# Performance work log

Hardware: AMD Instinct MI355X
Metric: run time of the kernel (lower is better)

## Reference

```python
import jax, jax.numpy as jnp
import numpy as np

HEAD_DIM = 128
ROPE_THETA = 10000.0


def _rope_cos_sin(positions, head_dim, theta):
    # positions: [T] int -> cos/sin [T, head_dim] (LLaMA half-split convention)
    inv_freq = 1.0 / (theta ** (jnp.arange(0, head_dim, 2, dtype=jnp.float32) / head_dim))
    ang = positions.astype(jnp.float32)[:, None] * inv_freq  # [T, D/2]
    cos = jnp.concatenate([jnp.cos(ang), jnp.cos(ang)], axis=-1)
    sin = jnp.concatenate([jnp.sin(ang), jnp.sin(ang)], axis=-1)
    return cos, sin


def _apply_rope(x, cos, sin):
    # x: [T, H, D]; rotate_half: (-x2, x1)
    half = x.shape[-1] // 2
    rot = jnp.concatenate([-x[..., half:], x[..., :half]], axis=-1)
    return x * cos[:, None, :] + rot * sin[:, None, :]


def setup_inputs() -> dict:
    key = jax.random.key(0)
    ks = jax.random.split(key, 5)
    T, hid = 4096, 4096
    S = 1024  # equal-length sequences -> B = T // S = 4
    Hq, Hk, D = 32, 8, HEAD_DIM
    hidden = jax.random.normal(ks[0], (T, hid), dtype=jnp.float32)
    positions = (jnp.arange(T, dtype=jnp.int32) % S)
    q_w = jax.random.normal(ks[1], (Hq * D, hid), dtype=jnp.float32) * 0.02
    k_w = jax.random.normal(ks[2], (Hk * D, hid), dtype=jnp.float32) * 0.02
    v_w = jax.random.normal(ks[3], (Hk * D, hid), dtype=jnp.float32) * 0.02
    o_w = jax.random.normal(ks[4], (hid, Hq * D), dtype=jnp.float32) * 0.02
    return {"hidden": hidden, "positions": positions, "q_w": q_w, "k_w": k_w,
            "v_w": v_w, "o_w": o_w, "seq_len": S}


def reference(hidden, positions, q_w, k_w, v_w, o_w, seq_len):
    T, hid = hidden.shape
    D = HEAD_DIM
    Hq = q_w.shape[0] // D
    Hk = k_w.shape[0] // D
    G = Hq // Hk  # num_kv_groups
    S = int(seq_len)
    B = T // S
    # QKV projections (ColumnParallel, tp=1): y = x @ W^T
    q = (hidden @ q_w.T).reshape(T, Hq, D)
    k = (hidden @ k_w.T).reshape(T, Hk, D)
    v = (hidden @ v_w.T).reshape(T, Hk, D)
    # fused RoPE on q and k
    cos, sin = _rope_cos_sin(positions, D, ROPE_THETA)
    q = _apply_rope(q, cos, sin)
    k = _apply_rope(k, cos, sin)
    # varlen (equal-length) causal GQA attention
    q = q.reshape(B, S, Hk, G, D)
    k = k.reshape(B, S, Hk, D)
    v = v.reshape(B, S, Hk, D)
    scale = 1.0 / np.sqrt(D).astype(np.float32)
    scores = jnp.einsum('bqhgd,bkhd->bhgqk', q, k) * scale  # [B,Hk,G,S,S]
    causal = jnp.tril(jnp.ones((S, S), dtype=bool))
    scores = jnp.where(causal, scores, jnp.asarray(-1e30, scores.dtype))
    attn = jax.nn.softmax(scores, axis=-1)
    out = jnp.einsum('bhgqk,bkhd->bqhgd', attn, v).reshape(T, Hq * D)
    # output projection (RowParallel, tp=1)
    return out @ o_w.T
```

## Files before the change

### kernel.cpp

```cpp
#include <hip/hip_runtime.h>
#include <hip/hip_bf16.h>

typedef __attribute__((ext_vector_type(8))) short bf16x8;
typedef __attribute__((ext_vector_type(4))) float f32x4;
typedef __attribute__((ext_vector_type(8))) unsigned short u16x8;

__device__ inline unsigned short f2bf(float f) {
  unsigned u = __builtin_bit_cast(unsigned, f);
  u += 0x7FFFu + ((u >> 16) & 1u);
  return (unsigned short)(u >> 16);
}
__device__ inline float b2f(unsigned short h) {
  unsigned u = ((unsigned)h) << 16;
  return __builtin_bit_cast(float, u);
}

typedef const __attribute__((address_space(1))) void* gas_ptr;
typedef __attribute__((address_space(3))) void* las_ptr;
__device__ inline void load_lds16(const void* g, void* l) {
  __builtin_amdgcn_global_load_lds((gas_ptr)g, (las_ptr)l, 16, 0, 0);
}

#define PHB() do { asm volatile("" ::: "memory"); __builtin_amdgcn_s_barrier(); \
                   __builtin_amdgcn_sched_barrier(0); } while (0)

__global__ __launch_bounds__(256) void cvt_f32_bf16(const float* __restrict__ src,
                                                    unsigned short* __restrict__ dst,
                                                    int n4) {
  int i = blockIdx.x * 256 + threadIdx.x;
  if (i >= n4) return;
  float4 v = ((const float4*)src)[i];
  ushort4 o;
  o.x = f2bf(v.x); o.y = f2bf(v.y); o.z = f2bf(v.z); o.w = f2bf(v.w);
  ((ushort4*)dst)[i] = o;
}

template <int NLOADS>
__device__ inline void stage_tile(const unsigned short* __restrict__ g, int ld,
                                  size_t grow0, int kcol0, char* ldsdst, int tid) {
#pragma unroll
  for (int i = 0; i < NLOADS; ++i) {
    int c = tid + i * 512;
    int r = c >> 3;
    int k = (c & 7) ^ (r & 7);
    load_lds16(g + (grow0 + r) * ld + kcol0 + k * 8, ldsdst + c * 16);
  }
}

__device__ inline void xcd_decode(int orig, int nTM, int nTN, int& bm, int& bn) {
  int x = orig & 7, i = orig >> 3;
  int xr = x >> 1, xc = x & 1;
  int bmch = nTM >> 2, bnch = nTN >> 1;
  bm = xr * bmch + i / bnch;
  bn = xc * bnch + i % bnch;
}

template <int Kc, int Nc, int Mc, bool OUT_F32>
__global__ __launch_bounds__(512, 1) void gemmT(const unsigned short* __restrict__ A,
                                                const unsigned short* __restrict__ B,
                                                void* __restrict__ Cv) {
  __shared__ __attribute__((aligned(16))) char lds[147456];
  const int tid = threadIdx.x;
  const int wave = tid >> 6, lane = tid & 63;
  const int l15 = lane & 15, l4 = lane >> 4;
  const int wr = wave >> 2, wc = wave & 3;
  int bm, bn;
  xcd_decode(blockIdx.x, Mc >> 7, Nc >> 8, bm, bn);
  const size_t rowA0 = (size_t)bm << 7, rowB0 = (size_t)bn << 8;
  const int nt = Kc >> 6;

  stage_tile<2>(A, Kc, rowA0, 0,  lds + 0,             tid);
  stage_tile<4>(B, Kc, rowB0, 0,  lds + 16384,         tid);
  stage_tile<2>(A, Kc, rowA0, 64, lds + 49152,         tid);
  stage_tile<4>(B, Kc, rowB0, 64, lds + 49152 + 16384, tid);
  asm volatile("s_waitcnt vmcnt(6)" ::: "memory");
  __builtin_amdgcn_s_barrier();
  __builtin_amdgcn_sched_barrier(0);

  f32x4 acc[4][4] = {};

#pragma unroll 3
  for (int t = 0; t < nt; ++t) {
    char* cbuf = lds + (t % 3) * 49152;
    char* sbuf = lds + ((t + 2) % 3) * 49152;
    const char* bufA = cbuf;
    const char* bufB = cbuf + 16384;
    const int kc2 = (t + 2) << 6;

    bf16x8 af[4][2], bf[4][2];

#pragma unroll
    for (int m = 0; m < 4; ++m) {
      int row = wr * 64 + m * 16 + l15;
#pragma unroll
      for (int kk = 0; kk < 2; ++kk)
        af[m][kk] = *(const bf16x8*)(bufA + (row << 7) + (((kk * 4 + l4) ^ (row & 7)) << 4));
    }
#pragma unroll
    for (int n = 0; n < 2; ++n) {
      int row = wc * 64 + n * 16 + l15;
#pragma unroll
      for (int kk = 0; kk < 2; ++kk)
        bf[n][kk] = *(const bf16x8*)(bufB + (row << 7) + (((kk * 4 + l4) ^ (row & 7)) << 4));
    }
    if (t < nt - 2) stage_tile<4>(B, Kc, rowB0, kc2, sbuf + 16384, tid);
    __builtin_amdgcn_s_barrier();
    asm volatile("s_waitcnt lgkmcnt(0)" ::: "memory");
    __builtin_amdgcn_sched_barrier(0);
    __builtin_amdgcn_s_setprio(1);
#pragma unroll
    for (int m = 0; m < 4; ++m)
#pragma unroll
      for (int n = 0; n < 2; ++n)
#pragma unroll
        for (int kk = 0; kk < 2; ++kk)
          acc[m][n] = __builtin_amdgcn_mfma_f32_16x16x32_bf16(af[m][kk], bf[n][kk], acc[m][n], 0, 0, 0);
    __builtin_amdgcn_s_setprio(0);
    PHB();

#pragma unroll
    for (int n = 2; n < 4; ++n) {
      int row = wc * 64 + n * 16 + l15;
#pragma unroll
      for (int kk = 0; kk < 2; ++kk)
        bf[n][kk] = *(const bf16x8*)(bufB + (row << 7) + (((kk * 4 + l4) ^ (row & 7)) << 4));
    }
    if (t < nt - 2) stage_tile<2>(A, Kc, rowA0, kc2, sbuf, tid);
    if (t <= nt - 3) { asm volatile("s_waitcnt vmcnt(6)" ::: "memory"); }
    else             { asm volatile("s_waitcnt vmcnt(0)" ::: "memory"); }
    __builtin_amdgcn_s_barrier();
    asm volatile("s_waitcnt lgkmcnt(0)" ::: "memory");
    __builtin_amdgcn_sched_barrier(0);
    __builtin_amdgcn_s_setprio(1);
#pragma unroll
    for (int m = 0; m < 4; ++m)
#pragma unroll
      for (int n = 2; n < 4; ++n)
#pragma unroll
        for (int kk = 0; kk < 2; ++kk)
          acc[m][n] = __builtin_amdgcn_mfma_f32_16x16x32_bf16(af[m][kk], bf[n][kk], acc[m][n], 0, 0, 0);
    __builtin_amdgcn_s_setprio(0);
    PHB();
  }

#pragma unroll
  for (int m = 0; m < 4; ++m)
#pragma unroll
    for (int n = 0; n < 4; ++n)
#pragma unroll
      for (int r = 0; r < 4; ++r) {
        size_t row = rowA0 + wr * 64 + m * 16 + l4 * 4 + r;
        size_t col = rowB0 + wc * 64 + n * 16 + l15;
        float v = acc[m][n][r];
        if (OUT_F32) ((float*)Cv)[row * Nc + col] = v;
        else         ((unsigned short*)Cv)[row * Nc + col] = f2bf(v);
      }
}

__global__ __launch_bounds__(256) void rope_kernel(unsigned short* __restrict__ qkv,
                                                   const int* __restrict__ positions) {
  int gw = (blockIdx.x * 256 + threadIdx.x) >> 6;
  int lane = threadIdx.x & 63;
  int t = gw / 40, h = gw % 40;
  size_t col0 = (h < 32) ? ((size_t)h << 7) : (4096 + ((size_t)(h - 32) << 7));
  unsigned short* p = qkv + (size_t)t * 6144 + col0;
  float pos = (float)positions[t];
  float inv = powf(10000.0f, -(float)lane * (1.0f / 64.0f));
  float ang = pos * inv;
  float s, c;
  sincosf(ang, &s, &c);
  float x1 = b2f(p[lane]);
  float x2 = b2f(p[lane + 64]);
  p[lane]      = f2bf(x1 * c - x2 * s);
  p[lane + 64] = f2bf(x2 * c + x1 * s);
}

__global__ __launch_bounds__(256, 4) void attn_kernel(const unsigned short* __restrict__ qkv,
                                                      unsigned short* __restrict__ ao) {
  int orig = blockIdx.x;
  int wgid = (orig & 7) * 128 + (orig >> 3);
  int pair = wgid & 7;
  int hq = (wgid >> 3) & 31;
  int b  = wgid >> 8;
  int hk = hq >> 2;
  int tid = threadIdx.x, wave = tid >> 6, lane = tid & 63;
  int l15 = lane & 15, l4 = lane >> 4;

  __shared__ __attribute__((aligned(16))) unsigned short Ks[64][128];
  __shared__ __attribute__((aligned(16))) unsigned short Vt[128][64];
  __shared__ __attribute__((aligned(16))) unsigned short Ps[4][16][64];

  const float scale = 0.08838834764831845f;

#pragma unroll 1
  for (int iq = 0; iq < 2; ++iq) {
    const int qa = iq ? (15 - pair) : pair;
    const size_t qrow0 = (size_t)(b * 1024 + qa * 64 + wave * 16);

    bf16x8 qf[4];
    {
      const unsigned short* qp = qkv + (qrow0 + l15) * 6144 + ((size_t)hq << 7) + l4 * 8;
#pragma unroll
      for (int kc = 0; kc < 4; ++kc) qf[kc] = *(const bf16x8*)(qp + kc * 32);
    }

    float m_i[4], l_i[4];
    f32x4 oacc[8];
#pragma unroll
    for (int r = 0; r < 4; ++r) { m_i[r] = -1e30f; l_i[r] = 0.0f; }
#pragma unroll
    for (int d = 0; d < 8; ++d) oacc[d] = f32x4{0.f, 0.f, 0.f, 0.f};

#pragma unroll 1
    for (int kt = 0; kt <= qa; ++kt) {
      __syncthreads();

      const unsigned short* kbase = qkv + (size_t)(b * 1024 + kt * 64) * 6144 + 4096 + ((size_t)hk << 7);
#pragma unroll
      for (int j = 0; j < 4; ++j) {
        int c = (j * 4 + wave) * 64 + lane;
        int r = c >> 4;
        int cc = (c & 15) ^ (r & 7);
        load_lds16(kbase + (size_t)r * 6144 + cc * 8, (char*)&Ks[0][0] + c * 16);
      }
      {
        const unsigned short* vp = qkv + (size_t)(b * 1024 + kt * 64 + lane) * 6144 + 5120 + ((size_t)hk << 7) + wave * 32;
        u16x8 va0 = *(const u16x8*)(vp);
        u16x8 va1 = *(const u16x8*)(vp + 8);
        u16x8 va2 = *(const u16x8*)(vp + 16);
        u16x8 va3 = *(const u16x8*)(vp + 24);
        int d0 = wave * 32;
#pragma unroll
        for (int c = 0; c < 8; ++c) {
          int sc = lane ^ ((c & 7) << 3);
          Vt[d0 + c][sc]      = va0[c];
          Vt[d0 + 8 + c][sc]  = va1[c];
          Vt[d0 + 16 + c][sc] = va2[c];
          Vt[d0 + 24 + c][sc] = va3[c];
        }
      }
      __syncthreads();

      float pbuf[4][4];
      float tmax[4] = {-1e30f, -1e30f, -1e30f, -1e30f};
#pragma unroll
      for (int nt = 0; nt < 4; ++nt) {
        f32x4 sacc = {0.f, 0.f, 0.f, 0.f};
        int row = nt * 16 + l15;
        __builtin_amdgcn_s_setprio(1);
#pragma unroll
        for (int kc = 0; kc < 4; ++kc) {
          const unsigned short* kp = &Ks[0][0] + row * 128 + (((kc * 4 + l4) ^ (row & 7)) * 8);
          bf16x8 kf = *(const bf16x8*)kp;
          sacc = __builtin_amdgcn_mfma_f32_16x16x32_bf16(qf[kc], kf, sacc, 0, 0, 0);
        }
        __builtin_amdgcn_s_setprio(0);
#pragma unroll
        for (int r = 0; r < 4; ++r) {
          float s = sacc[r] * scale;
          if (kt == qa) {
            int kcol = nt * 16 + l15;
            int qrow = wave * 16 + l4 * 4 + r;
            if (kcol > qrow) s = -1e30f;
          }
          pbuf[nt][r] = s;
          tmax[r] = fmaxf(tmax[r], s);
        }
      }

#pragma unroll
      for (int r = 0; r < 4; ++r) {
        float v = tmax[r];
        v = fmaxf(v, __shfl_xor(v, 1));
        v = fmaxf(v, __shfl_xor(v, 2));
        v = fmaxf(v, __shfl_xor(v, 4));
        v = fmaxf(v, __shfl_xor(v, 8));
        tmax[r] = v;
      }
      float rescale[4];
#pragma unroll
      for (int r = 0; r < 4; ++r) {
        float mn = fmaxf(m_i[r], tmax[r]);
        rescale[r] = __expf(m_i[r] - mn);
        m_i[r] = mn;
      }
      float psum[4] = {0.f, 0.f, 0.f, 0.f};
#pragma unroll
      for (int nt = 0; nt < 4; ++nt)
#pragma unroll
        for (int r = 0; r < 4; ++r) {
          float p = __expf(pbuf[nt][r] - m_i[r]);
          pbuf[nt][r] = p;
          psum[r] += p;
        }
#pragma unroll
      for (int r = 0; r < 4; ++r) {
        float v = psum[r];
        v += __shfl_xor(v, 1);
        v += __shfl_xor(v, 2);
        v += __shfl_xor(v, 4);
        v += __shfl_xor(v, 8);
        l_i[r] = l_i[r] * rescale[r] + v;
      }
#pragma unroll
      for (int d = 0; d < 8; ++d)
#pragma unroll
        for (int r = 0; r < 4; ++r) oacc[d][r] *= rescale[r];

#pragma unroll
      for (int nt = 0; nt < 4; ++nt)
#pragma unroll
        for (int r = 0; r < 4; ++r) {
          int r4 = l4 * 4 + r;
          Ps[wave][r4][(nt * 16 + l15) ^ ((r4 & 7) << 3)] = f2bf(pbuf[nt][r]);
        }

#pragma unroll
      for (int h = 0; h < 2; ++h) {
        bf16x8 pa = *(const bf16x8*)(&Ps[wave][0][0] + l15 * 64 + ((h * 32 + l4 * 8) ^ ((l15 & 7) << 3)));
        __builtin_amdgcn_s_setprio(1);
#pragma unroll
        for (int d = 0; d < 8; ++d) {
          int row = d * 16 + l15;
          bf16x8 vf = *(const bf16x8*)(&Vt[0][0] + row * 64 + ((h * 32 + l4 * 8) ^ ((row & 7) << 3)));
          oacc[d] = __builtin_amdgcn_mfma_f32_16x16x32_bf16(pa, vf, oacc[d], 0, 0, 0);
        }
        __builtin_amdgcn_s_setprio(0);
      }
    }

#pragma unroll
    for (int d = 0; d < 8; ++d)
#pragma unroll
      for (int r = 0; r < 4; ++r) {
        size_t row = qrow0 + l4 * 4 + r;
        size_t col = ((size_t)hq << 7) + d * 16 + l15;
        ao[row * 4096 + col] = f2bf(oacc[d][r] / l_i[r]);
      }
  }
}

extern "C" void kernel_launch(void* const* d_in, const int* in_sizes, int n_in,
                              void* d_out, int out_size, void* d_ws, size_t ws_size,
                              hipStream_t stream) {
  const float* hidden    = (const float*)d_in[0];
  const int*   positions = (const int*)d_in[1];
  const float* q_w       = (const float*)d_in[2];
  const float* k_w       = (const float*)d_in[3];
  const float* v_w       = (const float*)d_in[4];
  const float* o_w       = (const float*)d_in[5];
  float* out = (float*)d_out;

  char* ws = (char*)d_ws;
  unsigned short* hidB  = (unsigned short*)(ws);
  unsigned short* wqkvB = (unsigned short*)(ws + 33554432);
  unsigned short* woB   = (unsigned short*)(ws + 83886080);
  unsigned short* qkvB  = (unsigned short*)(ws + 117440512);
  unsigned short* aoB   = (unsigned short*)(ws + 167772160);

  cvt_f32_bf16<<<16384, 256, 0, stream>>>(hidden, hidB, 4194304);
  cvt_f32_bf16<<<16384, 256, 0, stream>>>(q_w, wqkvB, 4194304);
  cvt_f32_bf16<<<4096, 256, 0, stream>>>(k_w, wqkvB + 16777216, 1048576);
  cvt_f32_bf16<<<4096, 256, 0, stream>>>(v_w, wqkvB + 20971520, 1048576);
  cvt_f32_bf16<<<16384, 256, 0, stream>>>(o_w, woB, 4194304);

  gemmT<4096, 6144, 4096, false><<<768, 512, 0, stream>>>(hidB, wqkvB, (void*)qkvB);

  rope_kernel<<<40960, 256, 0, stream>>>(qkvB, positions);

  attn_kernel<<<1024, 256, 0, stream>>>(qkvB, aoB);

  gemmT<4096, 4096, 4096, true><<<512, 512, 0, stream>>>(aoB, woB, (void*)out);
}
```

Baseline: 549.3 us.

## Simplify GEMM main loop to single-phase with one barrier per K-tile

The GEMM loop drops its two-phase ping-pong schedule, which had two barriers per K-tile, explicit lgkmcnt waits, sched_barriers and setprio. It now issues both A and B prefetches for tile t+2 at the top of each iteration, loads all LDS fragments, runs all 32 MFMAs and uses a single barrier. The attention kernel also loses its setprio hints. This cuts synchronisation overhead and hands instruction scheduling back to the compiler, at the cost of the hand-tuned interleaving of LDS reads with MFMA work and the wave-priority control.

```diff
diff --git a/kernel.cpp b/kernel.cpp
--- a/kernel.cpp
+++ b/kernel.cpp
@@ -20,9 +20,6 @@
 __device__ inline void load_lds16(const void* g, void* l) {
   __builtin_amdgcn_global_load_lds((gas_ptr)g, (las_ptr)l, 16, 0, 0);
 }
-
-#define PHB() do { asm volatile("" ::: "memory"); __builtin_amdgcn_s_barrier(); \
-                   __builtin_amdgcn_sched_barrier(0); } while (0)
 
 __global__ __launch_bounds__(256) void cvt_f32_bf16(const float* __restrict__ src,
                                                     unsigned short* __restrict__ dst,
@@ -56,7 +53,7 @@
 }
 
 template <int Kc, int Nc, int Mc, bool OUT_F32>
-__global__ __launch_bounds__(512, 1) void gemmT(const unsigned short* __restrict__ A,
+__global__ __launch_bounds__(512, 1) void gemmP(const unsigned short* __restrict__ A,
                                                 const unsigned short* __restrict__ B,
                                                 void* __restrict__ Cv) {
   __shared__ __attribute__((aligned(16))) char lds[147456];
@@ -75,20 +72,22 @@
   stage_tile<4>(B, Kc, rowB0, 64, lds + 49152 + 16384, tid);
   asm volatile("s_waitcnt vmcnt(6)" ::: "memory");
   __builtin_amdgcn_s_barrier();
-  __builtin_amdgcn_sched_barrier(0);
 
   f32x4 acc[4][4] = {};
 
 #pragma unroll 3
   for (int t = 0; t < nt; ++t) {
-    char* cbuf = lds + (t % 3) * 49152;
+    const char* bufA = lds + (t % 3) * 49152;
+    const char* bufB = bufA + 16384;
     char* sbuf = lds + ((t + 2) % 3) * 49152;
-    const char* bufA = cbuf;
-    const char* bufB = cbuf + 16384;
     const int kc2 = (t + 2) << 6;
 
+    if (t < nt - 2) {
+      stage_tile<4>(B, Kc, rowB0, kc2, sbuf + 16384, tid);
+      stage_tile<2>(A, Kc, rowA0, kc2, sbuf, tid);
+    }
+
     bf16x8 af[4][2], bf[4][2];
-
 #pragma unroll
     for (int m = 0; m < 4; ++m) {
       int row = wr * 64 + m * 16 + l15;
@@ -97,50 +96,26 @@
         af[m][kk] = *(const bf16x8*)(bufA + (row << 7) + (((kk * 4 + l4) ^ (row & 7)) << 4));
     }
 #pragma unroll
-    for (int n = 0; n < 2; ++n) {
+    for (int n = 0; n < 4; ++n) {
       int row = wc * 64 + n * 16 + l15;
 #pragma unroll
       for (int kk = 0; kk < 2; ++kk)
         bf[n][kk] = *(const bf16x8*)(bufB + (row << 7) + (((kk * 4 + l4) ^ (row & 7)) << 4));
     }
-    if (t < nt - 2) stage_tile<4>(B, Kc, rowB0, kc2, sbuf + 16384, tid);
-    __builtin_amdgcn_s_barrier();
-    asm volatile("s_waitcnt lgkmcnt(0)" ::: "memory");
-    __builtin_amdgcn_sched_barrier(0);
-    __builtin_amdgcn_s_setprio(1);
+
 #pragma unroll
     for (int m = 0; m < 4; ++m)
 #pragma unroll
-      for (int n = 0; n < 2; ++n)
+      for (int n = 0; n < 4; ++n)
 #pragma unroll
         for (int kk = 0; kk < 2; ++kk)
           acc[m][n] = __builtin_amdgcn_mfma_f32_16x16x32_bf16(af[m][kk], bf[n][kk], acc[m][n], 0, 0, 0);
-    __builtin_amdgcn_s_setprio(0);
-    PHB();
-
-#pragma unroll
-    for (int n = 2; n < 4; ++n) {
-      int row = wc * 64 + n * 16 + l15;
-#pragma unroll
-      for (int kk = 0; kk < 2; ++kk)
-        bf[n][kk] = *(const bf16x8*)(bufB + (row << 7) + (((kk * 4 + l4) ^ (row & 7)) << 4));
-    }
-    if (t < nt - 2) stage_tile<2>(A, Kc, rowA0, kc2, sbuf, tid);
+
     if (t <= nt - 3) { asm volatile("s_waitcnt vmcnt(6)" ::: "memory"); }
     else             { asm volatile("s_waitcnt vmcnt(0)" ::: "memory"); }
+    asm volatile("" ::: "memory");
     __builtin_amdgcn_s_barrier();
-    asm volatile("s_waitcnt lgkmcnt(0)" ::: "memory");
-    __builtin_amdgcn_sched_barrier(0);
-    __builtin_amdgcn_s_setprio(1);
-#pragma unroll
-    for (int m = 0; m < 4; ++m)
-#pragma unroll
-      for (int n = 2; n < 4; ++n)
-#pragma unroll
-        for (int kk = 0; kk < 2; ++kk)
-          acc[m][n] = __builtin_amdgcn_mfma_f32_16x16x32_bf16(af[m][kk], bf[n][kk], acc[m][n], 0, 0, 0);
-    __builtin_amdgcn_s_setprio(0);
-    PHB();
+    asm volatile("" ::: "memory");
   }
 
 #pragma unroll
@@ -247,14 +222,12 @@
       for (int nt = 0; nt < 4; ++nt) {
         f32x4 sacc = {0.f, 0.f, 0.f, 0.f};
         int row = nt * 16 + l15;
-        __builtin_amdgcn_s_setprio(1);
 #pragma unroll
         for (int kc = 0; kc < 4; ++kc) {
           const unsigned short* kp = &Ks[0][0] + row * 128 + (((kc * 4 + l4) ^ (row & 7)) * 8);
           bf16x8 kf = *(const bf16x8*)kp;
           sacc = __builtin_amdgcn_mfma_f32_16x16x32_bf16(qf[kc], kf, sacc, 0, 0, 0);
         }
-        __builtin_amdgcn_s_setprio(0);
 #pragma unroll
         for (int r = 0; r < 4; ++r) {
           float s = sacc[r] * scale;
@@ -318,14 +291,12 @@
 #pragma unroll
       for (int h = 0; h < 2; ++h) {
         bf16x8 pa = *(const bf16x8*)(&Ps[wave][0][0] + l15 * 64 + ((h * 32 + l4 * 8) ^ ((l15 & 7) << 3)));
-        __builtin_amdgcn_s_setprio(1);
 #pragma unroll
         for (int d = 0; d < 8; ++d) {
           int row = d * 16 + l15;
           bf16x8 vf = *(const bf16x8*)(&Vt[0][0] + row * 64 + ((h * 32 + l4 * 8) ^ ((row & 7) << 3)));
           oacc[d] = __builtin_amdgcn_mfma_f32_16x16x32_bf16(pa, vf, oacc[d], 0, 0, 0);
         }
-        __builtin_amdgcn_s_setprio(0);
       }
     }
 
@@ -364,11 +335,11 @@
   cvt_f32_bf16<<<4096, 256, 0, stream>>>(v_w, wqkvB + 20971520, 1048576);
   cvt_f32_bf16<<<16384, 256, 0, stream>>>(o_w, woB, 4194304);
 
-  gemmT<4096, 6144, 4096, false><<<768, 512, 0, stream>>>(hidB, wqkvB, (void*)qkvB);
+  gemmP<4096, 6144, 4096, false><<<768, 512, 0, stream>>>(hidB, wqkvB, (void*)qkvB);
 
   rope_kernel<<<40960, 256, 0, stream>>>(qkvB, positions);
 
   attn_kernel<<<1024, 256, 0, stream>>>(qkvB, aoB);
 
-  gemmT<4096, 4096, 4096, true><<<512, 512, 0, stream>>>(aoB, woB, (void*)out);
-}
+  gemmP<4096, 4096, 4096, true><<<512, 512, 0, stream>>>(aoB, woB, (void*)out);
+}
```

Result: faster. 532.0 us (-3.1%).
